# Optimization experiments

Hardware: AMD Instinct MI355X
Metric: run time of the kernel (lower is better)

Reference implementation:

```python
import jax, jax.numpy as jnp
import numpy as np

B, T = 2097152, 32
EPS = 1e-07


def setup_inputs() -> dict:
    key = jax.random.key(0)
    k1, k2, k3 = jax.random.split(key, 3)
    logits = jax.random.normal(k1, (B, T), dtype=jnp.float32)
    time_bins = jax.random.randint(k2, (B,), 0, T, dtype=jnp.int64)
    events = jax.random.randint(k3, (B,), 0, 2, dtype=jnp.int32)
    return {"logits": logits, "time_bins": time_bins, "events": events}


def reference(logits, time_bins, events):
    Bn, Tn = logits.shape
    hazards = jax.nn.sigmoid(logits)                      # [B, T]
    t = jnp.clip(time_bins, 0, Tn - 1).astype(jnp.int32)  # [B]
    # sum of log(1 - h) over bins strictly before t (masked, vectorized)
    before = jnp.arange(Tn, dtype=jnp.int32)[None, :] < t[:, None]  # [B, T]
    log_one_minus = jnp.log(1.0 - hazards + EPS)
    log_surv = jnp.sum(jnp.where(before, log_one_minus, 0.0), axis=1)  # [B]
    # hazard at the event/censoring bin
    h_t = jnp.take_along_axis(hazards, t[:, None], axis=1)[:, 0]       # [B]
    term = jnp.where(events == 1,
                     jnp.log(h_t + EPS),
                     jnp.log(1.0 - h_t + EPS))
    loss = -(log_surv + term)  # [B]
    return jnp.mean(loss)      # reduction='mean'
```

## Files before the change

### kernel.cpp

```cpp
#include <hip/hip_runtime.h>


constexpr int T_BINS        = 32;
constexpr int BLOCK         = 256;
constexpr int LANES_PER_ROW = 8;
constexpr int ROWS_PER_ITER = BLOCK / LANES_PER_ROW;
constexpr int NBLOCKS       = 2048;

__global__ void dhl_detect_i64(const int* __restrict__ tb, int* __restrict__ flag) {
    __shared__ int s_any;
    if (threadIdx.x == 0) s_any = 0;
    __syncthreads();
    int v = tb[2 * threadIdx.x + 1];
    if (v != 0) atomicOr(&s_any, 1);
    __syncthreads();
    if (threadIdx.x == 0) *flag = (s_any == 0) ? 1 : 0;
}

__global__ __launch_bounds__(BLOCK) void dhl_main(
    const float4* __restrict__ logits4,
    const int*    __restrict__ tb,
    const int*    __restrict__ ev,
    const int*    __restrict__ flag64,
    float*        __restrict__ partials,
    int nrows, int rows_per_block)
{
    const int shift = *flag64;
    const int tid   = threadIdx.x;
    const int lane8 = tid & (LANES_PER_ROW - 1);
    const int rloc  = tid >> 3;
    const int j0    = lane8 * 4;
    const long long rbase = (long long)blockIdx.x * rows_per_block;

    float acc = 0.0f;
    for (int i = 0; i < rows_per_block; i += ROWS_PER_ITER) {
        long long row = rbase + i + rloc;
        if (row < nrows) {
            float4 v = logits4[row * LANES_PER_ROW + lane8];
            int t = tb[row << shift];
            t = min(max(t, 0), T_BINS - 1);
            const int e = ev[row];
            float xs[4] = {v.x, v.y, v.z, v.w};
            #pragma unroll
            for (int c = 0; c < 4; ++c) {
                float x = xs[c];
                float L = __logf(1.0f + __expf(x));
                int j = j0 + c;
                if (j <= t) acc -= L;
                if (j == t && e == 1) acc += x;
            }
        }
    }

    #pragma unroll
    for (int off = 32; off > 0; off >>= 1)
        acc += __shfl_down(acc, off, 64);

    __shared__ float sw[BLOCK / 64];
    if ((tid & 63) == 0) sw[tid >> 6] = acc;
    __syncthreads();
    if (tid == 0) {
        float s = 0.0f;
        #pragma unroll
        for (int w = 0; w < BLOCK / 64; ++w) s += sw[w];
        partials[blockIdx.x] = s;
    }
}

__global__ __launch_bounds__(BLOCK) void dhl_finalize(
    const float* __restrict__ partials, int n, float* __restrict__ out, float scale)
{
    const int tid = threadIdx.x;
    float acc = 0.0f;
    for (int i = tid; i < n; i += BLOCK) acc += partials[i];
    #pragma unroll
    for (int off = 32; off > 0; off >>= 1)
        acc += __shfl_down(acc, off, 64);
    __shared__ float sw[BLOCK / 64];
    if ((tid & 63) == 0) sw[tid >> 6] = acc;
    __syncthreads();
    if (tid == 0) {
        float s = 0.0f;
        #pragma unroll
        for (int w = 0; w < BLOCK / 64; ++w) s += sw[w];
        out[0] = s * scale;
    }
}

extern "C" void kernel_launch(void* const* d_in, const int* in_sizes, int n_in,
                              void* d_out, int out_size, void* d_ws, size_t ws_size,
                              hipStream_t stream) {
    const float4* logits4 = (const float4*)d_in[0];
    const int*    tb      = (const int*)d_in[1];
    const int*    ev      = (const int*)d_in[2];
    float*        out     = (float*)d_out;
    const int B = in_sizes[1];

    int*   flag     = (int*)d_ws;
    float* partials = (float*)((char*)d_ws + 256);

    int rows_per_block = (B + NBLOCKS - 1) / NBLOCKS;
    rows_per_block = ((rows_per_block + ROWS_PER_ITER - 1) / ROWS_PER_ITER) * ROWS_PER_ITER;
    int nblocks = (B + rows_per_block - 1) / rows_per_block;

    dhl_detect_i64<<<1, BLOCK, 0, stream>>>(tb, flag);
    dhl_main<<<nblocks, BLOCK, 0, stream>>>(logits4, tb, ev, flag, partials, B, rows_per_block);
    dhl_finalize<<<1, BLOCK, 0, stream>>>(partials, nblocks, out, -1.0f / (float)B);
}
```

Before: 59.90 us.

## Fuse detect, main and finalize into one kernel with last-block reduction

Each block now detects the int64 layout of time_bins itself with a wavefront ballot, which removes the separate detect kernel. The final reduction is done by the last block to finish, found through an atomic counter and threadfence, which removes the finalize kernel; a memset resets the counter before each launch. Logits are loaded with nontemporal hints to avoid polluting the cache. Launch overhead drops from three kernels to a memset plus one kernel, at the cost of an atomic per block and redundant probe loads.

```diff
diff --git a/kernel.cpp b/kernel.cpp
--- a/kernel.cpp
+++ b/kernel.cpp
@@ -1,5 +1,7 @@
 #include <hip/hip_runtime.h>
 
+
+typedef float vfloat4 __attribute__((ext_vector_type(4)));
 
 constexpr int T_BINS        = 32;
 constexpr int BLOCK         = 256;
@@ -7,26 +9,21 @@
 constexpr int ROWS_PER_ITER = BLOCK / LANES_PER_ROW;
 constexpr int NBLOCKS       = 2048;
 
-__global__ void dhl_detect_i64(const int* __restrict__ tb, int* __restrict__ flag) {
-    __shared__ int s_any;
-    if (threadIdx.x == 0) s_any = 0;
-    __syncthreads();
-    int v = tb[2 * threadIdx.x + 1];
-    if (v != 0) atomicOr(&s_any, 1);
-    __syncthreads();
-    if (threadIdx.x == 0) *flag = (s_any == 0) ? 1 : 0;
-}
+__global__ __launch_bounds__(BLOCK) void dhl_fused(
+    const vfloat4* __restrict__ logits4,
+    const int*     __restrict__ tb,
+    const int*     __restrict__ ev,
+    float*         __restrict__ partials,
+    unsigned int*  __restrict__ counter,
+    float*         __restrict__ out,
+    int nrows, int rows_per_block, int nblocks, float scale)
+{
+    const int tid  = threadIdx.x;
+    const int lane = tid & 63;
 
-__global__ __launch_bounds__(BLOCK) void dhl_main(
-    const float4* __restrict__ logits4,
-    const int*    __restrict__ tb,
-    const int*    __restrict__ ev,
-    const int*    __restrict__ flag64,
-    float*        __restrict__ partials,
-    int nrows, int rows_per_block)
-{
-    const int shift = *flag64;
-    const int tid   = threadIdx.x;
+    const int probe = tb[2 * lane + 1];
+    const int shift = (__ballot(probe != 0) == 0ULL) ? 1 : 0;
+
     const int lane8 = tid & (LANES_PER_ROW - 1);
     const int rloc  = tid >> 3;
     const int j0    = lane8 * 4;
@@ -36,14 +33,13 @@
     for (int i = 0; i < rows_per_block; i += ROWS_PER_ITER) {
         long long row = rbase + i + rloc;
         if (row < nrows) {
-            float4 v = logits4[row * LANES_PER_ROW + lane8];
+            vfloat4 v = __builtin_nontemporal_load(&logits4[row * LANES_PER_ROW + lane8]);
             int t = tb[row << shift];
             t = min(max(t, 0), T_BINS - 1);
             const int e = ev[row];
-            float xs[4] = {v.x, v.y, v.z, v.w};
             #pragma unroll
             for (int c = 0; c < 4; ++c) {
-                float x = xs[c];
+                float x = v[c];
                 float L = __logf(1.0f + __expf(x));
                 int j = j0 + c;
                 if (j <= t) acc -= L;
@@ -57,53 +53,49 @@
         acc += __shfl_down(acc, off, 64);
 
     __shared__ float sw[BLOCK / 64];
-    if ((tid & 63) == 0) sw[tid >> 6] = acc;
+    __shared__ bool  s_last;
+    if (lane == 0) sw[tid >> 6] = acc;
     __syncthreads();
+
     if (tid == 0) {
-        float s = 0.0f;
+        float s = sw[0] + sw[1] + sw[2] + sw[3];
+        partials[blockIdx.x] = s;
+        __threadfence();
+        unsigned old = atomicAdd(counter, 1u);
+        s_last = (old == (unsigned)(nblocks - 1));
+    }
+    __syncthreads();
+
+    if (s_last) {
+        __threadfence();
+        float a = 0.0f;
+        for (int i = tid; i < nblocks; i += BLOCK) a += partials[i];
         #pragma unroll
-        for (int w = 0; w < BLOCK / 64; ++w) s += sw[w];
-        partials[blockIdx.x] = s;
-    }
-}
-
-__global__ __launch_bounds__(BLOCK) void dhl_finalize(
-    const float* __restrict__ partials, int n, float* __restrict__ out, float scale)
-{
-    const int tid = threadIdx.x;
-    float acc = 0.0f;
-    for (int i = tid; i < n; i += BLOCK) acc += partials[i];
-    #pragma unroll
-    for (int off = 32; off > 0; off >>= 1)
-        acc += __shfl_down(acc, off, 64);
-    __shared__ float sw[BLOCK / 64];
-    if ((tid & 63) == 0) sw[tid >> 6] = acc;
-    __syncthreads();
-    if (tid == 0) {
-        float s = 0.0f;
-        #pragma unroll
-        for (int w = 0; w < BLOCK / 64; ++w) s += sw[w];
-        out[0] = s * scale;
+        for (int off = 32; off > 0; off >>= 1)
+            a += __shfl_down(a, off, 64);
+        if (lane == 0) sw[tid >> 6] = a;
+        __syncthreads();
+        if (tid == 0) out[0] = (sw[0] + sw[1] + sw[2] + sw[3]) * scale;
     }
 }
 
 extern "C" void kernel_launch(void* const* d_in, const int* in_sizes, int n_in,
                               void* d_out, int out_size, void* d_ws, size_t ws_size,
                               hipStream_t stream) {
-    const float4* logits4 = (const float4*)d_in[0];
-    const int*    tb      = (const int*)d_in[1];
-    const int*    ev      = (const int*)d_in[2];
-    float*        out     = (float*)d_out;
+    const vfloat4* logits4 = (const vfloat4*)d_in[0];
+    const int*     tb      = (const int*)d_in[1];
+    const int*     ev      = (const int*)d_in[2];
+    float*         out     = (float*)d_out;
     const int B = in_sizes[1];
 
-    int*   flag     = (int*)d_ws;
-    float* partials = (float*)((char*)d_ws + 256);
+    unsigned int* counter  = (unsigned int*)d_ws;
+    float*        partials = (float*)((char*)d_ws + 256);
 
     int rows_per_block = (B + NBLOCKS - 1) / NBLOCKS;
     rows_per_block = ((rows_per_block + ROWS_PER_ITER - 1) / ROWS_PER_ITER) * ROWS_PER_ITER;
     int nblocks = (B + rows_per_block - 1) / rows_per_block;
 
-    dhl_detect_i64<<<1, BLOCK, 0, stream>>>(tb, flag);
-    dhl_main<<<nblocks, BLOCK, 0, stream>>>(logits4, tb, ev, flag, partials, B, rows_per_block);
-    dhl_finalize<<<1, BLOCK, 0, stream>>>(partials, nblocks, out, -1.0f / (float)B);
+    (void)hipMemsetAsync(counter, 0, sizeof(unsigned int), stream);
+    dhl_fused<<<nblocks, BLOCK, 0, stream>>>(logits4, tb, ev, partials, counter, out,
+                                             B, rows_per_block, nblocks, -1.0f / (float)B);
 }
```

Result: slower. 148.5 us (+147.8%).
